# Optimization experiments

Measured on AMD Instinct MI355X. Metric: run time of the kernel, lower is better.

Reference implementation:

```python
import jax, jax.numpy as jnp
import numpy as np

MARGIN = 0.3
N_GALLERY = 32768
N_BATCH = 1024
D_EMB = 512
N_CLASSES = 1000


def setup_inputs() -> dict:
    key = jax.random.key(0)
    k1, k2, k3, k4 = jax.random.split(key, 4)
    inputs = jax.random.normal(k1, (N_BATCH, D_EMB), dtype=jnp.float32)
    features = jax.random.normal(k2, (N_GALLERY, D_EMB), dtype=jnp.float32)
    feat_labels = jax.random.randint(k3, (N_GALLERY,), 0, N_CLASSES, dtype=jnp.int64 if jax.config.read('jax_enable_x64') else jnp.int32)
    idx = jax.random.randint(k4, (N_BATCH,), 0, N_GALLERY, dtype=feat_labels.dtype)
    # invariant from the original code: idx[i] is in the positive set for targets[i]
    targets = feat_labels[idx]
    return {"inputs": inputs, "features": features, "targets": targets,
            "idx": idx, "feat_labels": feat_labels}


def reference(inputs, features, targets, idx, feat_labels):
    # sim_mat: [n, N] similarity against the gallery bank
    sim = jnp.einsum('nd,Nd->nN', inputs, features)
    n = targets.shape[0]
    # positives: same label in gallery, excluding the sample's own gallery slot
    pos_mask = targets[:, None] == feat_labels[None, :]          # [n, N]
    pos_mask = pos_mask.at[jnp.arange(n), idx].set(False)
    # negatives: every gallery entry with a different label
    neg_mask = targets[:, None] != feat_labels[None, :]          # [n, N]
    pos = jnp.min(jnp.where(pos_mask, sim, jnp.inf), axis=1)     # hardest positive (lowest sim)
    neg = jnp.max(jnp.where(neg_mask, sim, -jnp.inf), axis=1)    # hardest negative (highest sim)
    loss = jnp.maximum(neg - pos + MARGIN, 0.0)
    return jnp.mean(loss)
```

## Files before the change

kernel.cpp:

```cpp
#include <hip/hip_runtime.h>
#include <stdint.h>

#define MARGIN 0.3f
#define M 1024
#define NG 32768
#define K 512
#define BM 256
#define BN 256
#define BK 64
#define KT (K / BK)
#define NTILES (NG / BN)
#define MTILES (M / BM)
#define NPART (NTILES * 4)

typedef __attribute__((ext_vector_type(8))) __bf16 bf16x8;
typedef __attribute__((ext_vector_type(4))) float f32x4;
typedef unsigned short ushort_t;
typedef unsigned int uint_t;

#define BAR() __builtin_amdgcn_s_barrier()
#define SGB0() __builtin_amdgcn_sched_barrier(0)
#define WAIT_LGKM(n) asm volatile("s_waitcnt lgkmcnt(" #n ")" ::: "memory")
#define WAIT_VM0() asm volatile("s_waitcnt vmcnt(0)" ::: "memory")

static __device__ __forceinline__ ushort_t f2bf(float f) {
    uint_t u = __float_as_uint(f);
    u += 0x7FFFu + ((u >> 16) & 1u);
    return (ushort_t)(u >> 16);
}

__global__ __launch_bounds__(256) void cvt_kernel(const float* __restrict__ src,
                                                  ushort_t* __restrict__ dst, int n8) {
    int i = blockIdx.x * 256 + threadIdx.x;
    if (i >= n8) return;
    const float4* s4 = (const float4*)src;
    float4 a = s4[2 * i];
    float4 b = s4[2 * i + 1];
    uint4 o;
    o.x = (uint_t)f2bf(a.x) | ((uint_t)f2bf(a.y) << 16);
    o.y = (uint_t)f2bf(a.z) | ((uint_t)f2bf(a.w) << 16);
    o.z = (uint_t)f2bf(b.x) | ((uint_t)f2bf(b.y) << 16);
    o.w = (uint_t)f2bf(b.z) | ((uint_t)f2bf(b.w) << 16);
    ((uint4*)dst)[i] = o;
}

static __device__ __forceinline__ void gload_lds16(const void* gptr, void* lptr) {
    __builtin_amdgcn_global_load_lds(
        (const __attribute__((address_space(1))) uint32_t*)(gptr),
        (__attribute__((address_space(3))) uint32_t*)(uintptr_t)(lptr),
        16, 0, 0);
}

static __device__ __forceinline__ bf16x8 lds_read_b128(const ushort_t* p) {
    bf16x8 r;
    asm volatile("ds_read_b128 %0, %1"
                 : "=v"(r)
                 : "v"((const __attribute__((address_space(3))) ushort_t*)p));
    return r;
}

template <int CTRL>
static __device__ __forceinline__ float dpp_mv(float x) {
    return __int_as_float(__builtin_amdgcn_update_dpp(
        0, __float_as_int(x), CTRL, 0xF, 0xF, true));
}
static __device__ __forceinline__ float red16_min(float x) {
    x = fminf(x, dpp_mv<0xB1>(x));
    x = fminf(x, dpp_mv<0x4E>(x));
    x = fminf(x, dpp_mv<0x141>(x));
    x = fminf(x, dpp_mv<0x140>(x));
    return x;
}
static __device__ __forceinline__ float red16_max(float x) {
    x = fmaxf(x, dpp_mv<0xB1>(x));
    x = fmaxf(x, dpp_mv<0x4E>(x));
    x = fmaxf(x, dpp_mv<0x141>(x));
    x = fmaxf(x, dpp_mv<0x140>(x));
    return x;
}

__global__ __launch_bounds__(512, 2) void gemm_kernel(
    const ushort_t* __restrict__ A,
    const ushort_t* __restrict__ B,
    const int* __restrict__ targets,
    const int* __restrict__ idxv,
    const int* __restrict__ labels,
    float* __restrict__ pos_part,
    float* __restrict__ neg_part) {

    __shared__ __align__(16) ushort_t sA[2][BM * BK];
    __shared__ __align__(16) ushort_t sB[2][BN * BK];
    __shared__ int t_s[BM];
    __shared__ int i_s[BM];
    __shared__ int l_s[BN];

    const int tid = threadIdx.x;
    const int lane = tid & 63;
    const int w = tid >> 6;
    const int wm = w >> 2;
    const int wn = w & 3;
    const int l15 = lane & 15;
    const int lhi = lane >> 4;
    const int bid = blockIdx.x;
    const int ntile = bid & (NTILES - 1);
    const int mtile = bid >> 7;

    if (tid < BM) {
        t_s[tid] = targets[mtile * BM + tid];
        i_s[tid] = idxv[mtile * BM + tid];
    } else {
        l_s[tid - BM] = labels[ntile * BN + (tid - BM)];
    }

    f32x4 zero = {0.f, 0.f, 0.f, 0.f};
    f32x4 acc[8][4];
#pragma unroll
    for (int a = 0; a < 8; ++a)
#pragma unroll
        for (int b = 0; b < 4; ++b) acc[a][b] = zero;

    const int rstage = tid >> 3;
    const int cstage = (((tid & 7) ^ (rstage & 7)) << 3);
    const ushort_t* Abase = A + (size_t)mtile * BM * K;
    const ushort_t* Bbase = B + (size_t)ntile * BN * K;

    auto stage_half = [&](const ushort_t* g, ushort_t* l) {
        gload_lds16(g + (size_t)rstage * K + cstage, l + w * 512);
        gload_lds16(g + (size_t)(64 + rstage) * K + cstage, l + 4096 + w * 512);
    };
    auto stage_tile = [&](int buf, int kt) {
        stage_half(Abase + (size_t)kt * BK, &sA[buf][0]);
        stage_half(Abase + (size_t)kt * BK + (size_t)128 * K, &sA[buf][8192]);
        stage_half(Bbase + (size_t)kt * BK, &sB[buf][0]);
        stage_half(Bbase + (size_t)kt * BK + (size_t)128 * K, &sB[buf][8192]);
    };

    auto readA = [&](int buf, int mf, int kk) -> bf16x8 {
        const int r = wm * 128 + mf * 16 + l15;
        const int u = (kk * 4 + lhi) ^ (r & 7);
        return lds_read_b128(&sA[buf][r * 64 + u * 8]);
    };
    auto readB = [&](int buf, int nf, int kk) -> bf16x8 {
        const int r = wn * 64 + nf * 16 + l15;
        const int u = (kk * 4 + lhi) ^ (r & 7);
        return lds_read_b128(&sB[buf][r * 64 + u * 8]);
    };

    stage_tile(0, 0);
    WAIT_VM0();
    BAR();

#pragma unroll 1
    for (int kt = 0; kt < KT; ++kt) {
        const int cur = kt & 1;
        bf16x8 b0[4], a0lo[4], a0hi[4], b1[4], a1lo[4], a1hi[4];

#pragma unroll
        for (int nf = 0; nf < 4; ++nf) b0[nf] = readB(cur, nf, 0);
#pragma unroll
        for (int mf = 0; mf < 4; ++mf) a0lo[mf] = readA(cur, mf, 0);
#pragma unroll
        for (int mf = 0; mf < 4; ++mf) a0hi[mf] = readA(cur, mf + 4, 0);
#pragma unroll
        for (int nf = 0; nf < 4; ++nf) b1[nf] = readB(cur, nf, 1);

        if (kt + 1 < KT) stage_tile(cur ^ 1, kt + 1);

        WAIT_LGKM(8); SGB0();
        __builtin_amdgcn_s_setprio(1);
#pragma unroll
        for (int mf = 0; mf < 4; ++mf)
#pragma unroll
            for (int nf = 0; nf < 4; ++nf)
                acc[mf][nf] = __builtin_amdgcn_mfma_f32_16x16x32_bf16(a0lo[mf], b0[nf], acc[mf][nf], 0, 0, 0);
        __builtin_amdgcn_s_setprio(0);
        SGB0();

#pragma unroll
        for (int mf = 0; mf < 4; ++mf) a1lo[mf] = readA(cur, mf, 1);

        WAIT_LGKM(8); SGB0();
        __builtin_amdgcn_s_setprio(1);
#pragma unroll
        for (int mf = 0; mf < 4; ++mf)
#pragma unroll
            for (int nf = 0; nf < 4; ++nf)
                acc[mf + 4][nf] = __builtin_amdgcn_mfma_f32_16x16x32_bf16(a0hi[mf], b0[nf], acc[mf + 4][nf], 0, 0, 0);
        __builtin_amdgcn_s_setprio(0);
        SGB0();

#pragma unroll
        for (int mf = 0; mf < 4; ++mf) a1hi[mf] = readA(cur, mf + 4, 1);

        WAIT_LGKM(4); SGB0();
        __builtin_amdgcn_s_setprio(1);
#pragma unroll
        for (int mf = 0; mf < 4; ++mf)
#pragma unroll
            for (int nf = 0; nf < 4; ++nf)
                acc[mf][nf] = __builtin_amdgcn_mfma_f32_16x16x32_bf16(a1lo[mf], b1[nf], acc[mf][nf], 0, 0, 0);
        __builtin_amdgcn_s_setprio(0);
        SGB0();

        WAIT_LGKM(0); SGB0();
        __builtin_amdgcn_s_setprio(1);
#pragma unroll
        for (int mf = 0; mf < 4; ++mf)
#pragma unroll
            for (int nf = 0; nf < 4; ++nf)
                acc[mf + 4][nf] = __builtin_amdgcn_mfma_f32_16x16x32_bf16(a1hi[mf], b1[nf], acc[mf + 4][nf], 0, 0, 0);
        __builtin_amdgcn_s_setprio(0);
        SGB0();

        WAIT_VM0();
        BAR();
    }

    int labv[4], jv[4];
#pragma unroll
    for (int nf = 0; nf < 4; ++nf) {
        const int cl = wn * 64 + nf * 16 + l15;
        labv[nf] = l_s[cl];
        jv[nf] = ntile * BN + cl;
    }
#pragma unroll
    for (int mf = 0; mf < 8; ++mf) {
#pragma unroll
        for (int r = 0; r < 4; ++r) {
            const int row_l = wm * 128 + mf * 16 + lhi * 4 + r;
            const int tgt = t_s[row_l];
            const int exc = i_s[row_l];
            float pmin = INFINITY, nmax = -INFINITY;
#pragma unroll
            for (int nf = 0; nf < 4; ++nf) {
                const float v = acc[mf][nf][r];
                const bool same = (labv[nf] == tgt);
                pmin = fminf(pmin, (same && (jv[nf] != exc)) ? v : INFINITY);
                nmax = fmaxf(nmax, same ? -INFINITY : v);
            }
            pmin = red16_min(pmin);
            nmax = red16_max(nmax);
            if (l15 == 0) {
                const int row_g = mtile * BM + row_l;
                pos_part[(size_t)row_g * NPART + ntile * 4 + wn] = pmin;
                neg_part[(size_t)row_g * NPART + ntile * 4 + wn] = nmax;
            }
        }
    }
}

__global__ __launch_bounds__(256) void rowred_kernel(const float* __restrict__ pos_part,
                                                     const float* __restrict__ neg_part,
                                                     float* __restrict__ loss) {
    const int row = blockIdx.x;
    const int t = threadIdx.x;
    const float* pp = pos_part + (size_t)row * NPART;
    const float* nn = neg_part + (size_t)row * NPART;
    float p = fminf(pp[t], pp[t + 256]);
    float nx = fmaxf(nn[t], nn[t + 256]);
#pragma unroll
    for (int s = 1; s < 64; s <<= 1) {
        p = fminf(p, __shfl_xor(p, s, 64));
        nx = fmaxf(nx, __shfl_xor(nx, s, 64));
    }
    __shared__ float sp[4], sn[4];
    if ((t & 63) == 0) { sp[t >> 6] = p; sn[t >> 6] = nx; }
    __syncthreads();
    if (t == 0) {
        p = fminf(fminf(sp[0], sp[1]), fminf(sp[2], sp[3]));
        nx = fmaxf(fmaxf(sn[0], sn[1]), fmaxf(sn[2], sn[3]));
        const float l = nx - p + MARGIN;
        loss[row] = l > 0.f ? l : 0.f;
    }
}

__global__ __launch_bounds__(256) void final_kernel(const float* __restrict__ loss,
                                                    float* __restrict__ out) {
    const int t = threadIdx.x;
    float s = loss[t] + loss[t + 256] + loss[t + 512] + loss[t + 768];
#pragma unroll
    for (int sh = 1; sh < 64; sh <<= 1) s += __shfl_xor(s, sh, 64);
    __shared__ float sb[4];
    if ((t & 63) == 0) sb[t >> 6] = s;
    __syncthreads();
    if (t == 0) out[0] = (sb[0] + sb[1] + sb[2] + sb[3]) * (1.0f / 1024.0f);
}

extern "C" void kernel_launch(void* const* d_in, const int* in_sizes, int n_in,
                              void* d_out, int out_size, void* d_ws, size_t ws_size,
                              hipStream_t stream) {
    const float* inputs = (const float*)d_in[0];
    const float* features = (const float*)d_in[1];
    const int* targets = (const int*)d_in[2];
    const int* idxv = (const int*)d_in[3];
    const int* labels = (const int*)d_in[4];

    char* ws = (char*)d_ws;
    ushort_t* A = (ushort_t*)ws;
    ushort_t* B = (ushort_t*)(ws + (1u << 20));
    float* pos_part = (float*)(ws + (1u << 20) + (32u << 20));
    float* neg_part = pos_part + (size_t)M * NPART;
    float* loss = neg_part + (size_t)M * NPART;

    cvt_kernel<<<(NG * K / 8) / 256, 256, 0, stream>>>(features, B, NG * K / 8);
    cvt_kernel<<<(M * K / 8) / 256, 256, 0, stream>>>(inputs, A, M * K / 8);

    gemm_kernel<<<MTILES * NTILES, 512, 0, stream>>>(A, B, targets, idxv, labels,
                                                     pos_part, neg_part);

    rowred_kernel<<<M, 256, 0, stream>>>(pos_part, neg_part, loss);
    final_kernel<<<1, 256, 0, stream>>>(loss, (float*)d_out);
}
```

Baseline: 152.1 us.

## Deepen GEMM load pipeline to two tiles ahead and fuse final reductions

The GEMM main loop now prefetches two K-tiles ahead instead of one. The next-next tile's global-to-LDS loads are issued mid-iteration after an extra barrier, and a partial vmcnt wait lets one tile's loads stay in flight across iterations. The row reduction and mean kernels are merged into one 16-block kernel that atomically accumulates into the output, which the input conversion kernel zeroes first. This removes a launch and hides more memory latency, at the cost of an extra barrier per iteration and reliance on exact vmcnt counts for correctness.

```diff
diff --git a/kernel.cpp b/kernel.cpp
--- a/kernel.cpp
+++ b/kernel.cpp
@@ -21,7 +21,7 @@
 #define BAR() __builtin_amdgcn_s_barrier()
 #define SGB0() __builtin_amdgcn_sched_barrier(0)
 #define WAIT_LGKM(n) asm volatile("s_waitcnt lgkmcnt(" #n ")" ::: "memory")
-#define WAIT_VM0() asm volatile("s_waitcnt vmcnt(0)" ::: "memory")
+#define WAIT_VM(n) asm volatile("s_waitcnt vmcnt(" #n ")" ::: "memory")
 
 static __device__ __forceinline__ ushort_t f2bf(float f) {
     uint_t u = __float_as_uint(f);
@@ -30,8 +30,10 @@
 }
 
 __global__ __launch_bounds__(256) void cvt_kernel(const float* __restrict__ src,
-                                                  ushort_t* __restrict__ dst, int n8) {
+                                                  ushort_t* __restrict__ dst, int n8,
+                                                  float* __restrict__ out_zero) {
     int i = blockIdx.x * 256 + threadIdx.x;
+    if (out_zero && i == 0) out_zero[0] = 0.f;
     if (i >= n8) return;
     const float4* s4 = (const float4*)src;
     float4 a = s4[2 * i];
@@ -147,7 +149,8 @@
     };
 
     stage_tile(0, 0);
-    WAIT_VM0();
+    stage_tile(1, 1);
+    WAIT_VM(8);
     BAR();
 
 #pragma unroll 1
@@ -164,8 +167,6 @@
 #pragma unroll
         for (int nf = 0; nf < 4; ++nf) b1[nf] = readB(cur, nf, 1);
 
-        if (kt + 1 < KT) stage_tile(cur ^ 1, kt + 1);
-
         WAIT_LGKM(8); SGB0();
         __builtin_amdgcn_s_setprio(1);
 #pragma unroll
@@ -203,6 +204,12 @@
         SGB0();
 
         WAIT_LGKM(0); SGB0();
+
+        if (kt + 2 < KT) {
+            BAR();
+            stage_tile(cur, kt + 2);
+        }
+
         __builtin_amdgcn_s_setprio(1);
 #pragma unroll
         for (int mf = 0; mf < 4; ++mf)
@@ -212,8 +219,10 @@
         __builtin_amdgcn_s_setprio(0);
         SGB0();
 
-        WAIT_VM0();
-        BAR();
+        if (kt < KT - 1) {
+            if (kt + 2 < KT) { WAIT_VM(8); } else { WAIT_VM(0); }
+            BAR();
+        }
     }
 
     int labv[4], jv[4];
@@ -249,41 +258,38 @@
     }
 }
 
-__global__ __launch_bounds__(256) void rowred_kernel(const float* __restrict__ pos_part,
+__global__ __launch_bounds__(256) void finish_kernel(const float* __restrict__ pos_part,
                                                      const float* __restrict__ neg_part,
-                                                     float* __restrict__ loss) {
-    const int row = blockIdx.x;
-    const int t = threadIdx.x;
-    const float* pp = pos_part + (size_t)row * NPART;
-    const float* nn = neg_part + (size_t)row * NPART;
-    float p = fminf(pp[t], pp[t + 256]);
-    float nx = fmaxf(nn[t], nn[t + 256]);
-#pragma unroll
-    for (int s = 1; s < 64; s <<= 1) {
-        p = fminf(p, __shfl_xor(p, s, 64));
-        nx = fmaxf(nx, __shfl_xor(nx, s, 64));
-    }
-    __shared__ float sp[4], sn[4];
-    if ((t & 63) == 0) { sp[t >> 6] = p; sn[t >> 6] = nx; }
+                                                     float* __restrict__ out) {
+    const int tid = threadIdx.x;
+    const int lane = tid & 63;
+    const int wv = tid >> 6;
+    const int gwave = blockIdx.x * 4 + wv;
+    float lsum = 0.f;
+#pragma unroll 1
+    for (int rr = 0; rr < 16; ++rr) {
+        const int row = gwave * 16 + rr;
+        const float* pp = pos_part + (size_t)row * NPART;
+        const float* nn = neg_part + (size_t)row * NPART;
+        float p = INFINITY, nx = -INFINITY;
+#pragma unroll
+        for (int j = 0; j < 8; ++j) {
+            p = fminf(p, pp[lane + j * 64]);
+            nx = fmaxf(nx, nn[lane + j * 64]);
+        }
+#pragma unroll
+        for (int s = 1; s < 64; s <<= 1) {
+            p = fminf(p, __shfl_xor(p, s, 64));
+            nx = fmaxf(nx, __shfl_xor(nx, s, 64));
+        }
+        const float l = nx - p + MARGIN;
+        lsum += l > 0.f ? l : 0.f;
+    }
+    __shared__ float sb[4];
+    if (lane == 0) sb[wv] = lsum;
     __syncthreads();
-    if (t == 0) {
-        p = fminf(fminf(sp[0], sp[1]), fminf(sp[2], sp[3]));
-        nx = fmaxf(fmaxf(sn[0], sn[1]), fmaxf(sn[2], sn[3]));
-        const float l = nx - p + MARGIN;
-        loss[row] = l > 0.f ? l : 0.f;
-    }
-}
-
-__global__ __launch_bounds__(256) void final_kernel(const float* __restrict__ loss,
-                                                    float* __restrict__ out) {
-    const int t = threadIdx.x;
-    float s = loss[t] + loss[t + 256] + loss[t + 512] + loss[t + 768];
-#pragma unroll
-    for (int sh = 1; sh < 64; sh <<= 1) s += __shfl_xor(s, sh, 64);
-    __shared__ float sb[4];
-    if ((t & 63) == 0) sb[t >> 6] = s;
-    __syncthreads();
-    if (t == 0) out[0] = (sb[0] + sb[1] + sb[2] + sb[3]) * (1.0f / 1024.0f);
+    if (tid == 0)
+        atomicAdd(out, (sb[0] + sb[1] + sb[2] + sb[3]) * (1.0f / (float)M));
 }
 
 extern "C" void kernel_launch(void* const* d_in, const int* in_sizes, int n_in,
@@ -300,14 +306,12 @@
     ushort_t* B = (ushort_t*)(ws + (1u << 20));
     float* pos_part = (float*)(ws + (1u << 20) + (32u << 20));
     float* neg_part = pos_part + (size_t)M * NPART;
-    float* loss = neg_part + (size_t)M * NPART;
-
-    cvt_kernel<<<(NG * K / 8) / 256, 256, 0, stream>>>(features, B, NG * K / 8);
-    cvt_kernel<<<(M * K / 8) / 256, 256, 0, stream>>>(inputs, A, M * K / 8);
+
+    cvt_kernel<<<(NG * K / 8) / 256, 256, 0, stream>>>(features, B, NG * K / 8, nullptr);
+    cvt_kernel<<<(M * K / 8) / 256, 256, 0, stream>>>(inputs, A, M * K / 8, (float*)d_out);
 
     gemm_kernel<<<MTILES * NTILES, 512, 0, stream>>>(A, B, targets, idxv, labels,
                                                      pos_part, neg_part);
 
-    rowred_kernel<<<M, 256, 0, stream>>>(pos_part, neg_part, loss);
-    final_kernel<<<1, 256, 0, stream>>>(loss, (float*)d_out);
-}
+    finish_kernel<<<16, 256, 0, stream>>>(pos_part, neg_part, (float*)d_out);
+}
```

Result: slower. 160.8 us (+5.7%).
